# Kernel tuning notes

Measured on AMD Instinct MI355X. Metric: run time of the kernel, lower is better.

The kernel has to match this reference:

```python
import jax, jax.numpy as jnp
import numpy as np


def setup_inputs() -> dict:
    key = jax.random.key(0)
    k1, k2 = jax.random.split(key)
    preds = jax.random.normal(k1, (8, 4096, 3), dtype=jnp.float32)
    gts = jax.random.normal(k2, (8, 4096, 3), dtype=jnp.float32)
    return {"preds": preds, "gts": gts}


def reference(preds, gts):
    # P[b, i, j] = ||gts[b,i]||^2 + ||preds[b,j]||^2 - 2 * gts[b,i] . preds[b,j]
    x, y = gts, preds
    rx = jnp.sum(x * x, axis=-1)               # [b, Nx]
    ry = jnp.sum(y * y, axis=-1)               # [b, Ny]
    zz = jnp.einsum('bnd,bmd->bnm', x, y)      # [b, Nx, Ny]
    P = rx[:, :, None] + ry[:, None, :] - 2.0 * zz
    loss_1 = jnp.sum(jnp.min(P, axis=1), axis=1)  # min over gts points, sum over preds
    loss_2 = jnp.sum(jnp.min(P, axis=2), axis=1)  # min over preds points, sum over gts
    return loss_1 + loss_2                        # [b]
```

## Files before the change

kernel.cpp:

```cpp
#include <hip/hip_runtime.h>
#include <float.h>

#define NPTS 4096
#define NB   8

typedef __bf16 bf16x8 __attribute__((ext_vector_type(8)));
typedef float  f32x16 __attribute__((ext_vector_type(16)));

__device__ __forceinline__ float min3f(float a, float b, float c) {
    return fminf(fminf(a, b), c);
}

__device__ __forceinline__ void split_bf(float v, __bf16& hi, __bf16& lo) {
    hi = (__bf16)v;
    lo = (__bf16)(v - (float)hi);
}

__global__ void __launch_bounds__(256, 4) chamfer_mfma(
    const float* __restrict__ preds,
    const float* __restrict__ gts,
    float* __restrict__ part)
{
    __shared__ __align__(16) __bf16 Btab[2][512][8];
    __shared__ float pmLds[4][512];

    const int rowgrp = blockIdx.x >> 3;
    const int jgroup = blockIdx.x & 7;
    const int bdir   = blockIdx.y;
    const int b = bdir >> 1, dir = bdir & 1;

    const float* rows = ((dir == 0) ? gts   : preds) + (size_t)b * NPTS * 3;
    const float* cols = ((dir == 0) ? preds : gts)   + (size_t)b * NPTS * 3;

    const int tid  = threadIdx.x;
    const int lane = tid & 63;
    const int w    = tid >> 6;
    const __bf16 one = (__bf16)1.0f, zero = (__bf16)0.0f;

    #pragma unroll
    for (int r = 0; r < 2; ++r) {
        const int c = tid + r * 256;
        const float* p = cols + (size_t)(jgroup * 512 + c) * 3;
        const float x = p[0], y = p[1], z = p[2];
        const float h = x * x + y * y + z * z;
        __bf16 uh, ul, vh, vl, wh, wl, hh, hl;
        split_bf(-2.0f * x, uh, ul);
        split_bf(-2.0f * y, vh, vl);
        split_bf(-2.0f * z, wh, wl);
        split_bf(h, hh, hl);
        bf16x8 b0, b1;
        b0[0] = uh; b0[1] = ul; b0[2] = uh; b0[3] = vh;
        b0[4] = vl; b0[5] = vh; b0[6] = wh; b0[7] = wl;
        b1[0] = wh; b1[1] = one; b1[2] = one; b1[3] = hh;
        b1[4] = hl; b1[5] = zero; b1[6] = zero; b1[7] = zero;
        *(bf16x8*)&Btab[0][c][0] = b0;
        *(bf16x8*)&Btab[1][c][0] = b1;
    }

    bf16x8 afr[4];
    const int rbase = rowgrp * 512 + w * 128;
    #pragma unroll
    for (int ib = 0; ib < 4; ++ib) {
        const float* g = rows + (size_t)(rbase + ib * 32 + (lane & 31)) * 3;
        const float x = g[0], y = g[1], z = g[2];
        const float h = x * x + y * y + z * z;
        __bf16 xh, xl, yh, yl, zh, zl, hh, hl;
        split_bf(x, xh, xl);
        split_bf(y, yh, yl);
        split_bf(z, zh, zl);
        split_bf(h, hh, hl);
        bf16x8 a;
        if (lane < 32) {
            a[0] = xh; a[1] = xh; a[2] = xl; a[3] = yh;
            a[4] = yh; a[5] = yl; a[6] = zh; a[7] = zh;
        } else {
            a[0] = zl; a[1] = hh; a[2] = hl; a[3] = one;
            a[4] = one; a[5] = zero; a[6] = zero; a[7] = zero;
        }
        afr[ib] = a;
    }
    __syncthreads();

    f32x16 zc = 0.0f;

    for (int jt = 0; jt < 16; ++jt) {
        const bf16x8 bfr = *(const bf16x8*)&Btab[lane >> 5][jt * 32 + (lane & 31)][0];
        float pmin = FLT_MAX;
        #pragma unroll
        for (int ib = 0; ib < 4; ++ib) {
            f32x16 d = __builtin_amdgcn_mfma_f32_32x32x16_bf16(afr[ib], bfr, zc, 0, 0, 0);
            const float m0 = min3f(d[0],  d[1],  d[2]);
            const float m1 = min3f(d[3],  d[4],  d[5]);
            const float m2 = min3f(d[6],  d[7],  d[8]);
            const float m3 = min3f(d[9],  d[10], d[11]);
            const float m4 = min3f(d[12], d[13], d[14]);
            const float mm = min3f(min3f(m0, m1, m2), fminf(m3, m4), d[15]);
            pmin = fminf(pmin, mm);
        }
        pmin = fminf(pmin, __shfl_xor(pmin, 32, 64));
        if (lane < 32) pmLds[w][jt * 32 + (lane & 31)] = pmin;
    }
    __syncthreads();

    float* wsout = part + (size_t)(bdir * 8 + rowgrp) * NPTS + jgroup * 512;
    #pragma unroll
    for (int r = 0; r < 2; ++r) {
        const int idx = tid + r * 256;
        const float m = fminf(min3f(pmLds[0][idx], pmLds[1][idx], pmLds[2][idx]),
                              pmLds[3][idx]);
        wsout[idx] = m;
    }
}

__global__ void __launch_bounds__(256) chamfer_comb(
    const float* __restrict__ part, float* __restrict__ out)
{
    const int blk  = blockIdx.x;
    const int bdir = blk >> 2, quarter = blk & 3;
    const int tid  = threadIdx.x;
    const float* p0 = part + (size_t)bdir * 8 * NPTS;

    float sum = 0.0f;
    #pragma unroll
    for (int c = 0; c < 4; ++c) {
        const int col = quarter * 1024 + c * 256 + tid;
        float m = FLT_MAX;
        #pragma unroll
        for (int band = 0; band < 8; ++band)
            m = fminf(m, p0[(size_t)band * NPTS + col]);
        sum += m;
    }

    __shared__ float red[256];
    red[tid] = sum;
    __syncthreads();
    #pragma unroll
    for (int off = 128; off >= 1; off >>= 1) {
        if (tid < off) red[tid] += red[tid + off];
        __syncthreads();
    }
    if (tid == 0) atomicAdd(&out[bdir >> 1], red[0]);
}

extern "C" void kernel_launch(void* const* d_in, const int* in_sizes, int n_in,
                              void* d_out, int out_size, void* d_ws, size_t ws_size,
                              hipStream_t stream)
{
    const float* preds = (const float*)d_in[0];
    const float* gts   = (const float*)d_in[1];
    float* out  = (float*)d_out;
    float* part = (float*)d_ws;

    hipMemsetAsync(d_out, 0, NB * sizeof(float), stream);
    chamfer_mfma<<<dim3(64, 16), 256, 0, stream>>>(preds, gts, part);
    chamfer_comb<<<64, 256, 0, stream>>>(part, out);
}
```

Baseline: 24.32 us.

## Fuse combine kernel into main kernel via last-block atomic tickets

Removes the separate combine kernel launch. Each block takes an atomic ticket per (batch,direction,column group), and the last of the 8 row-group blocks reduces the partial minima and sums them. A second ticket per batch lets the last of 16 finishers write the final output. This saves one kernel launch and its tail, at the cost of threadfences and atomics in every block and a serialized tail reduction in a few blocks.

```diff
diff --git a/kernel.cpp b/kernel.cpp
--- a/kernel.cpp
+++ b/kernel.cpp
@@ -16,13 +16,18 @@
     lo = (__bf16)(v - (float)hi);
 }
 
-__global__ void __launch_bounds__(256, 4) chamfer_mfma(
+__global__ void __launch_bounds__(256, 4) chamfer_fused(
     const float* __restrict__ preds,
     const float* __restrict__ gts,
-    float* __restrict__ part)
+    float* __restrict__ part,
+    float* __restrict__ ws2,
+    int*   __restrict__ cnt1,
+    int*   __restrict__ cntB,
+    float* __restrict__ out)
 {
     __shared__ __align__(16) __bf16 Btab[2][512][8];
     __shared__ float pmLds[4][512];
+    __shared__ int ticket;
 
     const int rowgrp = blockIdx.x >> 3;
     const int jgroup = blockIdx.x & 7;
@@ -106,40 +111,49 @@
     #pragma unroll
     for (int r = 0; r < 2; ++r) {
         const int idx = tid + r * 256;
-        const float m = fminf(min3f(pmLds[0][idx], pmLds[1][idx], pmLds[2][idx]),
-                              pmLds[3][idx]);
-        wsout[idx] = m;
-    }
-}
-
-__global__ void __launch_bounds__(256) chamfer_comb(
-    const float* __restrict__ part, float* __restrict__ out)
-{
-    const int blk  = blockIdx.x;
-    const int bdir = blk >> 2, quarter = blk & 3;
-    const int tid  = threadIdx.x;
-    const float* p0 = part + (size_t)bdir * 8 * NPTS;
-
-    float sum = 0.0f;
-    #pragma unroll
-    for (int c = 0; c < 4; ++c) {
-        const int col = quarter * 1024 + c * 256 + tid;
-        float m = FLT_MAX;
-        #pragma unroll
-        for (int band = 0; band < 8; ++band)
-            m = fminf(m, p0[(size_t)band * NPTS + col]);
-        sum += m;
+        wsout[idx] = fminf(min3f(pmLds[0][idx], pmLds[1][idx], pmLds[2][idx]),
+                           pmLds[3][idx]);
     }
 
-    __shared__ float red[256];
-    red[tid] = sum;
+    __threadfence();
     __syncthreads();
-    #pragma unroll
-    for (int off = 128; off >= 1; off >>= 1) {
-        if (tid < off) red[tid] += red[tid + off];
+    if (tid == 0) ticket = atomicAdd(&cnt1[bdir * 8 + jgroup], 1);
+    __syncthreads();
+
+    if (ticket == 7) {
+        __threadfence();
+        const float* p0 = part + (size_t)bdir * 8 * NPTS + jgroup * 512;
+        float sum = 0.0f;
+        #pragma unroll
+        for (int r = 0; r < 2; ++r) {
+            const int col = tid + r * 256;
+            float m = p0[col];
+            #pragma unroll
+            for (int band = 1; band < 8; ++band)
+                m = fminf(m, p0[(size_t)band * NPTS + col]);
+            sum += m;
+        }
+        float* red = &pmLds[0][0];
+        red[tid] = sum;
         __syncthreads();
+        #pragma unroll
+        for (int off = 128; off >= 1; off >>= 1) {
+            if (tid < off) red[tid] += red[tid + off];
+            __syncthreads();
+        }
+        if (tid == 0) {
+            ws2[b * 16 + dir * 8 + jgroup] = red[0];
+            __threadfence();
+            const int t2 = atomicAdd(&cntB[b], 1);
+            if (t2 == 15) {
+                __threadfence();
+                float s = 0.0f;
+                #pragma unroll
+                for (int i = 0; i < 16; ++i) s += ws2[b * 16 + i];
+                out[b] = s;
+            }
+        }
     }
-    if (tid == 0) atomicAdd(&out[bdir >> 1], red[0]);
 }
 
 extern "C" void kernel_launch(void* const* d_in, const int* in_sizes, int n_in,
@@ -149,9 +163,13 @@
     const float* preds = (const float*)d_in[0];
     const float* gts   = (const float*)d_in[1];
     float* out  = (float*)d_out;
+
     float* part = (float*)d_ws;
+    float* ws2  = part + (size_t)16 * 8 * NPTS;
+    int*   cnt1 = (int*)(ws2 + 128);
+    int*   cntB = cnt1 + 128;
 
-    hipMemsetAsync(d_out, 0, NB * sizeof(float), stream);
-    chamfer_mfma<<<dim3(64, 16), 256, 0, stream>>>(preds, gts, part);
-    chamfer_comb<<<64, 256, 0, stream>>>(part, out);
+    hipMemsetAsync(cnt1, 0, (128 + 8) * sizeof(int), stream);
+    chamfer_fused<<<dim3(64, 16), 256, 0, stream>>>(preds, gts, part, ws2,
+                                                    cnt1, cntB, out);
 }
```

Measured after the change: 91.42 us. 3.76x slower.

## Fuse combine kernel into MFMA kernel by giving each block all rows

Applied to the files above, without the earlier changes.

Each block now covers all 4096 rows (8 waves x 512 rows, 16 A fragments per wave) for a 256-column chunk. It computes the full column minima in-block and reduces their sum directly with an atomicAdd, which removes the partial-result workspace and the second combine kernel launch. The cost is a grid of only 256 blocks of 512 threads and much higher register use from 16 fragments plus a fully unrolled loop. That may lower occupancy and latency hiding on a GPU with many CUs.

```diff
diff --git a/kernel.cpp b/kernel.cpp
--- a/kernel.cpp
+++ b/kernel.cpp
@@ -16,17 +16,17 @@
     lo = (__bf16)(v - (float)hi);
 }
 
-__global__ void __launch_bounds__(256, 4) chamfer_mfma(
+__global__ void __launch_bounds__(512, 2) chamfer_fused(
     const float* __restrict__ preds,
     const float* __restrict__ gts,
-    float* __restrict__ part)
+    float* __restrict__ out)
 {
-    __shared__ __align__(16) __bf16 Btab[2][512][8];
-    __shared__ float pmLds[4][512];
+    __shared__ __align__(16) __bf16 Btab[2][256][8];
+    __shared__ float pmLds[8][256];
+    __shared__ float red[256];
 
-    const int rowgrp = blockIdx.x >> 3;
-    const int jgroup = blockIdx.x & 7;
-    const int bdir   = blockIdx.y;
+    const int chunk = blockIdx.x;
+    const int bdir  = blockIdx.y;
     const int b = bdir >> 1, dir = bdir & 1;
 
     const float* rows = ((dir == 0) ? gts   : preds) + (size_t)b * NPTS * 3;
@@ -37,10 +37,9 @@
     const int w    = tid >> 6;
     const __bf16 one = (__bf16)1.0f, zero = (__bf16)0.0f;
 
-    #pragma unroll
-    for (int r = 0; r < 2; ++r) {
-        const int c = tid + r * 256;
-        const float* p = cols + (size_t)(jgroup * 512 + c) * 3;
+    if (tid < 256) {
+        const int c = tid;
+        const float* p = cols + (size_t)(chunk * 256 + c) * 3;
         const float x = p[0], y = p[1], z = p[2];
         const float h = x * x + y * y + z * z;
         __bf16 uh, ul, vh, vl, wh, wl, hh, hl;
@@ -57,10 +56,10 @@
         *(bf16x8*)&Btab[1][c][0] = b1;
     }
 
-    bf16x8 afr[4];
-    const int rbase = rowgrp * 512 + w * 128;
+    bf16x8 afr[16];
+    const int rbase = w * 512;
     #pragma unroll
-    for (int ib = 0; ib < 4; ++ib) {
+    for (int ib = 0; ib < 16; ++ib) {
         const float* g = rows + (size_t)(rbase + ib * 32 + (lane & 31)) * 3;
         const float x = g[0], y = g[1], z = g[2];
         const float h = x * x + y * y + z * z;
@@ -83,11 +82,12 @@
 
     f32x16 zc = 0.0f;
 
-    for (int jt = 0; jt < 16; ++jt) {
+    #pragma unroll
+    for (int jt = 0; jt < 8; ++jt) {
         const bf16x8 bfr = *(const bf16x8*)&Btab[lane >> 5][jt * 32 + (lane & 31)][0];
         float pmin = FLT_MAX;
         #pragma unroll
-        for (int ib = 0; ib < 4; ++ib) {
+        for (int ib = 0; ib < 16; ++ib) {
             f32x16 d = __builtin_amdgcn_mfma_f32_32x32x16_bf16(afr[ib], bfr, zc, 0, 0, 0);
             const float m0 = min3f(d[0],  d[1],  d[2]);
             const float m1 = min3f(d[3],  d[4],  d[5]);
@@ -102,44 +102,19 @@
     }
     __syncthreads();
 
-    float* wsout = part + (size_t)(bdir * 8 + rowgrp) * NPTS + jgroup * 512;
-    #pragma unroll
-    for (int r = 0; r < 2; ++r) {
-        const int idx = tid + r * 256;
-        const float m = fminf(min3f(pmLds[0][idx], pmLds[1][idx], pmLds[2][idx]),
-                              pmLds[3][idx]);
-        wsout[idx] = m;
+    if (tid < 256) {
+        float m = pmLds[0][tid];
+        #pragma unroll
+        for (int q = 1; q < 8; ++q) m = fminf(m, pmLds[q][tid]);
+        red[tid] = m;
     }
-}
-
-__global__ void __launch_bounds__(256) chamfer_comb(
-    const float* __restrict__ part, float* __restrict__ out)
-{
-    const int blk  = blockIdx.x;
-    const int bdir = blk >> 2, quarter = blk & 3;
-    const int tid  = threadIdx.x;
-    const float* p0 = part + (size_t)bdir * 8 * NPTS;
-
-    float sum = 0.0f;
-    #pragma unroll
-    for (int c = 0; c < 4; ++c) {
-        const int col = quarter * 1024 + c * 256 + tid;
-        float m = FLT_MAX;
-        #pragma unroll
-        for (int band = 0; band < 8; ++band)
-            m = fminf(m, p0[(size_t)band * NPTS + col]);
-        sum += m;
-    }
-
-    __shared__ float red[256];
-    red[tid] = sum;
     __syncthreads();
     #pragma unroll
     for (int off = 128; off >= 1; off >>= 1) {
         if (tid < off) red[tid] += red[tid + off];
         __syncthreads();
     }
-    if (tid == 0) atomicAdd(&out[bdir >> 1], red[0]);
+    if (tid == 0) atomicAdd(&out[b], red[0]);
 }
 
 extern "C" void kernel_launch(void* const* d_in, const int* in_sizes, int n_in,
@@ -148,10 +123,8 @@
 {
     const float* preds = (const float*)d_in[0];
     const float* gts   = (const float*)d_in[1];
-    float* out  = (float*)d_out;
-    float* part = (float*)d_ws;
+    float* out = (float*)d_out;
 
     hipMemsetAsync(d_out, 0, NB * sizeof(float), stream);
-    chamfer_mfma<<<dim3(64, 16), 256, 0, stream>>>(preds, gts, part);
-    chamfer_comb<<<64, 256, 0, stream>>>(part, out);
+    chamfer_fused<<<dim3(16, 16), 512, 0, stream>>>(preds, gts, out);
 }
```

Result: no change. 24.49 us (+0.7%).
